# Kernel tuning notes

Measured on AMD Instinct MI355X. Metric: run time of the kernel, lower is better.

Reference implementation:

```python
import jax, jax.numpy as jnp
import numpy as np

B, T, R = 256, 20, 100          # batch, decode steps, image regions
IN_DIM, NUM_HID, V_DIM = 300, 1024, 2048
VOCAB = 10000


def _p(key, shape, scale=0.02):
    return (jax.random.normal(key, shape, dtype=jnp.float32) * scale)


def setup_inputs() -> dict:
    key = jax.random.key(0)
    ks = jax.random.split(key, 24)
    H4 = 4 * NUM_HID
    return {
        "caption": jax.random.randint(ks[0], (B, T - 1), 0, VOCAB),
        "features": jax.random.normal(ks[1], (B, R, V_DIM), dtype=jnp.float32),
        # word embedding table
        "emb": _p(ks[2], (VOCAB, IN_DIM)),
        # v_input: Linear(v_dim, in_dim)
        "W_vin": _p(ks[3], (V_DIM, IN_DIM)), "b_vin": jnp.zeros((IN_DIM,), jnp.float32),
        # rnn_v: LSTMCell(in_dim + num_hid + v_dim, num_hid); weights stored [in, 4H]
        "W_ih_v": _p(ks[4], (IN_DIM + NUM_HID + V_DIM, H4)),
        "W_hh_v": _p(ks[5], (NUM_HID, H4)),
        "b_v": jnp.zeros((H4,), jnp.float32),
        # attention MLP
        "W_va": _p(ks[6], (V_DIM, NUM_HID)), "b_va": jnp.zeros((NUM_HID,), jnp.float32),
        "W_ha": _p(ks[7], (NUM_HID, NUM_HID)), "b_ha": jnp.zeros((NUM_HID,), jnp.float32),
        "W_a": _p(ks[8], (NUM_HID, 1)), "b_a": jnp.zeros((1,), jnp.float32),
        # rnn_c: LSTMCell(num_hid + v_dim, num_hid)
        "W_ih_c": _p(ks[9], (NUM_HID + V_DIM, H4)),
        "W_hh_c": _p(ks[10], (NUM_HID, H4)),
        "b_c": jnp.zeros((H4,), jnp.float32),
        # classifier: Linear(num_hid, vocab)
        "W_cls": _p(ks[11], (NUM_HID, VOCAB)), "b_cls": jnp.zeros((VOCAB,), jnp.float32),
    }


def _lstm_cell(x, h, c, W_ih, W_hh, b):
    # torch LSTMCell gate order: i, f, g, o
    g = x @ W_ih + h @ W_hh + b
    i, f, gg, o = jnp.split(g, 4, axis=-1)
    c2 = jax.nn.sigmoid(f) * c + jax.nn.sigmoid(i) * jnp.tanh(gg)
    h2 = jax.nn.sigmoid(o) * jnp.tanh(c2)
    return h2, c2


def reference(caption, features, emb, W_vin, b_vin, W_ih_v, W_hh_v, b_v,
              W_va, b_va, W_ha, b_ha, W_a, b_a, W_ih_c, W_hh_c, b_c,
              W_cls, b_cls):
    cap_emb = emb[caption]                                  # [B, T-1, in_dim]
    feat_mean = jnp.mean(features, axis=1)                  # [B, v_dim]
    v_rnn_inp = feat_mean @ W_vin + b_vin                   # [B, in_dim]
    x = jnp.concatenate([v_rnn_inp[:, None, :], cap_emb], axis=1)  # [B, T, in_dim]
    # precompute region projection (loop-invariant in the original)
    va = features @ W_va + b_va                             # [B, R, num_hid]

    def step(carry, x_t):
        h_v, c_v, h_c, c_c = carry
        inp_v = jnp.concatenate([feat_mean, h_c, x_t], axis=1)
        h_v, c_v = _lstm_cell(inp_v, h_v, c_v, W_ih_v, W_hh_v, b_v)
        ha = h_v @ W_ha + b_ha                              # [B, num_hid]
        att_logit = jnp.tanh(va + ha[:, None, :]) @ W_a + b_a  # [B, R, 1]
        att = jax.nn.softmax(att_logit, axis=1)             # softmax over regions
        feat_hat = jnp.mean(features * att, axis=1)         # [B, v_dim] (mean, as in torch)
        inp_c = jnp.concatenate([feat_hat, h_v], axis=1)
        h_c, c_c = _lstm_cell(inp_c, h_c, c_c, W_ih_c, W_hh_c, b_c)
        return (h_v, c_v, h_c, c_c), (h_c, att)

    z = jnp.zeros((x.shape[0], NUM_HID), jnp.float32)
    _, (outs, atts) = jax.lax.scan(step, (z, z, z, z), jnp.swapaxes(x, 0, 1))
    outputs = jnp.swapaxes(outs, 0, 1)                      # [B, T, num_hid]
    attention = jnp.swapaxes(atts, 0, 1)                    # [B, T, R, 1]
    repr_ = outputs @ W_cls + b_cls                         # [B, T, vocab]
    return repr_, attention
```

## Files before the change

kernel.cpp:

```cpp
#include <hip/hip_runtime.h>
#include <math.h>

namespace {

constexpr int NB  = 256;
constexpr int NT  = 20;
constexpr int NR  = 100;
constexpr int IND = 300;
constexpr int NH  = 1024;
constexpr int VD  = 2048;
constexpr int H4  = 4096;
constexpr int VOC = 10000;
constexpr int VOCP = 10112;

constexpr int KGV = 4704;  constexpr int KGVO = 2352;
constexpr int KGC = 8192;  constexpr int KGCO = 4096;
constexpr int KHA = 2048;  constexpr int KHAO = 1024;
constexpr int KCL = 2048;  constexpr int KCLO = 1024;
constexpr int KFM = 4096;  constexpr int KFMO = 2048;
constexpr int NVI = 384;
constexpr int A2VLD = 4096;
constexpr int X2LD  = 608;

constexpr int ZGV = 8;  constexpr int KSV = 608;
constexpr int ZGC = 8;  constexpr int KSC = 1024;
constexpr int ZHA = 16; constexpr int KSH = 128;
constexpr int ZFM = 8;  constexpr int KSF = 512;

typedef short  s8v  __attribute__((ext_vector_type(8)));
typedef float  f4v  __attribute__((ext_vector_type(4)));

__device__ __forceinline__ float sigm(float x) { return 1.f / (1.f + expf(-x)); }
__device__ __forceinline__ unsigned short f2b(float x) {
  return __builtin_bit_cast(unsigned short, (__bf16)x);
}
__device__ __forceinline__ float b2f(unsigned short u) {
  return (float)__builtin_bit_cast(__bf16, u);
}
__device__ __forceinline__ int Frow(int row) { return (row ^ (row >> 2)) & 3; }
__device__ __forceinline__ void storeCK(unsigned short* rowbase, int segkp, int korig,
                                        float x, int Fs) {
  const unsigned short h = f2b(x);
  const unsigned short l = f2b(x - b2f(h));
  const int ph = segkp + ((korig >> 3) << 4) + (korig & 7);
  rowbase[ph ^ Fs] = h;
  rowbase[(ph + 8) ^ Fs] = l;
}

__device__ __forceinline__ void gload16(const unsigned short* g, unsigned short* l) {
  __builtin_amdgcn_global_load_lds(
      (const __attribute__((address_space(1))) void*)g,
      (__attribute__((address_space(3))) void*)l, 16, 0, 0);
}

#define BARRIER()  __syncthreads()
#define VMWAIT0()  asm volatile("s_waitcnt vmcnt(0)" ::: "memory")

template<bool OUT_BF16, bool DUPB>
__global__ __launch_bounds__(256)
void gemm128(const unsigned short* __restrict__ A, int lda,
             const unsigned short* __restrict__ Bt, int ldb,
             void* __restrict__ Cv, int ldc,
             const float* __restrict__ bias,
             int N, int Kp)
{
  __shared__ unsigned short As[2][128 * 32];
  __shared__ unsigned short Bs[2][128 * 32];
  const int tid = threadIdx.x, wid = tid >> 6, lane = tid & 63;
  const int wm = (wid >> 1) * 64, wn = (wid & 1) * 64;
  const int m0 = blockIdx.x * 128, n0 = blockIdx.y * 128;
  const int sr = tid >> 2, sc = (tid & 3) * 8;
  const unsigned short* a0 = A + (size_t)(m0 + sr) * lda + sc;
  const unsigned short* a1 = a0 + (size_t)64 * lda;
  const unsigned short* bsrcD = Bt + (size_t)(n0 + (tid >> 1)) * ldb + (tid & 1) * 8;
  const unsigned short* b0 = Bt + (size_t)(n0 + sr) * ldb + sc;
  const unsigned short* b1 = b0 + (size_t)64 * ldb;
  const int rr = lane & 15;
  const int kc = (((lane >> 4) ^ Frow(rr)) & 3) * 8;
  const int wrow = tid >> 1, wc8 = tid & 1;
  const int wF = Frow(wrow & 15);

  f4v acc[4][4] = {};

  auto stageA = [&](int s, int k) {
    gload16(a0 + k, &As[s][tid * 8]);
    gload16(a1 + k, &As[s][2048 + tid * 8]);
  };
  auto stageBplain = [&](int s, int k) {
    gload16(b0 + k, &Bs[s][tid * 8]);
    gload16(b1 + k, &Bs[s][2048 + tid * 8]);
  };
  auto writeBdup = [&](int s, s8v v) {
    *(s8v*)&Bs[s][wrow * 32 + (((2 * wc8) ^ wF) * 8)] = v;
    *(s8v*)&Bs[s][wrow * 32 + (((2 * wc8 + 1) ^ wF) * 8)] = v;
  };
  auto compute = [&](int s) {
    s8v a[4], b[4];
#pragma unroll
    for (int i = 0; i < 4; ++i) a[i] = *(const s8v*)&As[s][(wm + i * 16 + rr) * 32 + kc];
#pragma unroll
    for (int j = 0; j < 4; ++j) b[j] = *(const s8v*)&Bs[s][(wn + j * 16 + rr) * 32 + kc];
#pragma unroll
    for (int i = 0; i < 4; ++i)
#pragma unroll
      for (int j = 0; j < 4; ++j)
        acc[i][j] = __builtin_amdgcn_mfma_f32_16x16x32_bf16(a[i], b[j], acc[i][j], 0, 0, 0);
  };

  stageA(0, 0);
  if constexpr (DUPB) {
    s8v v = *(const s8v*)(bsrcD);
    VMWAIT0();
    writeBdup(0, v);
  } else {
    stageBplain(0, 0);
    VMWAIT0();
  }
  BARRIER();

  int cur = 0;
  for (int k0 = 0; k0 < Kp; k0 += 32) {
    const bool more = (k0 + 32 < Kp);
    if constexpr (DUPB) {
      s8v v;
      if (more) { stageA(cur ^ 1, k0 + 32); v = *(const s8v*)(bsrcD + ((k0 + 32) >> 1)); }
      compute(cur);
      VMWAIT0();
      if (more) writeBdup(cur ^ 1, v);
    } else {
      if (more) { stageA(cur ^ 1, k0 + 32); stageBplain(cur ^ 1, k0 + 32); }
      compute(cur);
      VMWAIT0();
    }
    BARRIER();
    cur ^= 1;
  }

  const int cr = (lane >> 4) * 4, cc = lane & 15;
#pragma unroll
  for (int i = 0; i < 4; ++i) {
#pragma unroll
    for (int j = 0; j < 4; ++j) {
      const int gn = n0 + wn + j * 16 + cc;
      if (gn >= N) continue;
#pragma unroll
      for (int r = 0; r < 4; ++r) {
        const int gm = m0 + wm + i * 16 + cr + r;
        float v = acc[i][j][r] + bias[gn];
        if constexpr (OUT_BF16) ((unsigned short*)Cv)[(size_t)gm * ldc + gn] = f2b(v);
        else                    ((float*)Cv)[(size_t)gm * ldc + gn] = v;
      }
    }
  }
}

template<bool XSEG>
__global__ __launch_bounds__(256)
void gemm_sk2(const unsigned short* __restrict__ A, int lda,
              const unsigned short* __restrict__ X2, int t,
              const unsigned short* __restrict__ Bt, int ldb,
              float* __restrict__ P, int N, int Kp, int Ksplit)
{
  __shared__ unsigned short As[2][128 * 32];
  __shared__ unsigned short Bs[2][128 * 32];
  const int tid = threadIdx.x, wid = tid >> 6, lane = tid & 63;
  const int wm = (wid >> 1) * 64, wn = (wid & 1) * 64;
  const int m0 = blockIdx.y * 128, n0 = blockIdx.x * 128;
  const int kbeg = blockIdx.z * Ksplit;
  const int kend = min(Kp, kbeg + Ksplit);
  const int sr = tid >> 2, sc = (tid & 3) * 8;
  const unsigned short* a0 = A + (size_t)(m0 + sr) * lda + sc;
  const unsigned short* a1 = a0 + (size_t)64 * lda;
  const unsigned short* x0 = nullptr;
  const unsigned short* x1 = nullptr;
  if constexpr (XSEG) {
    x0 = X2 + ((size_t)(m0 + sr) * NT + t) * X2LD + sc;
    x1 = x0 + (size_t)64 * NT * X2LD;
  }
  const unsigned short* bsrcD = Bt + (size_t)(n0 + (tid >> 1)) * ldb + (tid & 1) * 8;
  const int rr = lane & 15;
  const int kc = (((lane >> 4) ^ Frow(rr)) & 3) * 8;
  const int wrow = tid >> 1, wc8 = tid & 1;
  const int wF = Frow(wrow & 15);

  f4v acc[4][4] = {};

  auto stageA = [&](int s, int k) {
    if constexpr (XSEG) {
      if (k >= A2VLD) {
        gload16(x0 + (k - A2VLD), &As[s][tid * 8]);
        gload16(x1 + (k - A2VLD), &As[s][2048 + tid * 8]);
      } else {
        gload16(a0 + k, &As[s][tid * 8]);
        gload16(a1 + k, &As[s][2048 + tid * 8]);
      }
    } else {
      gload16(a0 + k, &As[s][tid * 8]);
      gload16(a1 + k, &As[s][2048 + tid * 8]);
    }
  };
  auto writeBdup = [&](int s, s8v v) {
    *(s8v*)&Bs[s][wrow * 32 + (((2 * wc8) ^ wF) * 8)] = v;
    *(s8v*)&Bs[s][wrow * 32 + (((2 * wc8 + 1) ^ wF) * 8)] = v;
  };
  auto compute = [&](int s) {
    s8v a[4], b[4];
#pragma unroll
    for (int i = 0; i < 4; ++i) a[i] = *(const s8v*)&As[s][(wm + i * 16 + rr) * 32 + kc];
#pragma unroll
    for (int j = 0; j < 4; ++j) b[j] = *(const s8v*)&Bs[s][(wn + j * 16 + rr) * 32 + kc];
#pragma unroll
    for (int i = 0; i < 4; ++i)
#pragma unroll
      for (int j = 0; j < 4; ++j)
        acc[i][j] = __builtin_amdgcn_mfma_f32_16x16x32_bf16(a[i], b[j], acc[i][j], 0, 0, 0);
  };

  stageA(0, kbeg);
  {
    s8v v = *(const s8v*)(bsrcD + (kbeg >> 1));
    VMWAIT0();
    writeBdup(0, v);
  }
  BARRIER();

  int cur = 0;
  for (int k0 = kbeg; k0 < kend; k0 += 32) {
    const bool more = (k0 + 32 < kend);
    s8v v;
    if (more) { stageA(cur ^ 1, k0 + 32); v = *(const s8v*)(bsrcD + ((k0 + 32) >> 1)); }
    compute(cur);
    VMWAIT0();
    if (more) writeBdup(cur ^ 1, v);
    BARRIER();
    cur ^= 1;
  }

  float* out = P + (size_t)blockIdx.z * 256 * N;
  const int cr = (lane >> 4) * 4, cc = lane & 15;
#pragma unroll
  for (int i = 0; i < 4; ++i)
#pragma unroll
    for (int j = 0; j < 4; ++j)
#pragma unroll
      for (int r = 0; r < 4; ++r)
        out[(size_t)(m0 + wm + i * 16 + cr + r) * N + n0 + wn + j * 16 + cc] = acc[i][j][r];
}

__global__ __launch_bounds__(256)
void gemm_va_f32(const float* __restrict__ A, int lda,
                 const unsigned short* __restrict__ Bt, int ldb,
                 unsigned short* __restrict__ C, int ldc,
                 const float* __restrict__ bias, int N, int Kp)
{
  __shared__ unsigned short As[128 * 32];
  __shared__ unsigned short Bs[128 * 32];
  const int tid = threadIdx.x, wid = tid >> 6, lane = tid & 63;
  const int wm = (wid >> 1) * 64, wn = (wid & 1) * 64;
  const int m0 = blockIdx.x * 128, n0 = blockIdx.y * 128;
  const unsigned short* bsrc0 = Bt + (size_t)(n0 + (tid >> 2)) * ldb + (tid & 3) * 8;
  const unsigned short* bsrc1 = bsrc0 + (size_t)64 * ldb;
  const int rr = lane & 15;
  const int kc = (((lane >> 4) ^ Frow(rr)) & 3) * 8;

  f4v acc[4][4] = {};
  for (int k0 = 0; k0 < Kp; k0 += 32) {
#pragma unroll
    for (int it = 0; it < 4; ++it) {
      const int r = it * 32 + (tid >> 3), c = (tid & 7) * 4;
      const float4 v = *(const float4*)(A + (size_t)(m0 + r) * lda + k0 + c);
      ushort4 w;
      w.x = f2b(v.x); w.y = f2b(v.y); w.z = f2b(v.z); w.w = f2b(v.w);
      *(ushort4*)&As[r * 32 + (c ^ (Frow(r & 15) << 3))] = w;
    }
    gload16(bsrc0 + k0, &Bs[tid * 8]);
    gload16(bsrc1 + k0, &Bs[2048 + tid * 8]);
    __syncthreads();
    s8v a[4], b[4];
#pragma unroll
    for (int i = 0; i < 4; ++i) a[i] = *(const s8v*)&As[(wm + i * 16 + rr) * 32 + kc];
#pragma unroll
    for (int j = 0; j < 4; ++j) b[j] = *(const s8v*)&Bs[(wn + j * 16 + rr) * 32 + kc];
#pragma unroll
    for (int i = 0; i < 4; ++i)
#pragma unroll
      for (int j = 0; j < 4; ++j)
        acc[i][j] = __builtin_amdgcn_mfma_f32_16x16x32_bf16(a[i], b[j], acc[i][j], 0, 0, 0);
    __syncthreads();
  }
  const int cr = (lane >> 4) * 4, cc = lane & 15;
#pragma unroll
  for (int i = 0; i < 4; ++i)
#pragma unroll
    for (int j = 0; j < 4; ++j) {
      const int gn = n0 + wn + j * 16 + cc;
      if (gn >= N) continue;
#pragma unroll
      for (int r = 0; r < 4; ++r)
        C[(size_t)(m0 + wm + i * 16 + cr + r) * ldc + gn] = f2b(acc[i][j][r] + bias[gn]);
    }
}

__global__ void convB_k(const float* __restrict__ src, int srcld, int K, int N,
                        unsigned short* __restrict__ dst, int dstld, int coff, int mode)
{
  __shared__ float t[32][33];
  const int kb = blockIdx.x * 32, nb = blockIdx.y * 32;
  const int tx = threadIdx.x & 31, ty = threadIdx.x >> 5;
#pragma unroll
  for (int i = 0; i < 32; i += 8) {
    const int k = kb + ty + i, n = nb + tx;
    t[ty + i][tx] = (k < K && n < N) ? src[(size_t)k * srcld + n] : 0.f;
  }
  __syncthreads();
#pragma unroll
  for (int i = 0; i < 32; i += 8) {
    const int n = nb + ty + i, k = kb + tx;
    if (n >= N || k >= K) continue;
    const float x = t[tx][ty + i];
    unsigned short* row = dst + (size_t)n * dstld;
    if (mode == 0) {
      row[coff + k] = f2b(x);
    } else {
      row[(coff + k) ^ (Frow(n & 15) << 3)] = f2b(x);
    }
  }
}

__global__ void zpad_plain_k(unsigned short* __restrict__ dst, int ld, int c0, int N)
{
  const int w = ld - c0;
  const int idx = blockIdx.x * 256 + threadIdx.x;
  if (idx >= N * w) return;
  dst[(size_t)(idx / w) * ld + c0 + (idx % w)] = 0;
}

__global__ void zfill_k(unsigned short* __restrict__ p, int n)
{
  const int i = blockIdx.x * 256 + threadIdx.x;
  if (i < n) p[i] = 0;
}

__global__ void feat_pass_k(const float* __restrict__ feat, float* __restrict__ fm,
                            unsigned short* __restrict__ f16out)
{
  const int idx = blockIdx.x * 256 + threadIdx.x;
  if (idx >= NB * (VD / 8)) return;
  const int d0 = (idx & (VD / 8 - 1)) * 8, b = idx / (VD / 8);
  const float* base = feat + (size_t)b * NR * VD + d0;
  float s[8] = {};
  for (int r = 0; r < NR; ++r) {
    const float4 x0 = *(const float4*)(base + (size_t)r * VD);
    const float4 x1 = *(const float4*)(base + (size_t)r * VD + 4);
    s[0] += x0.x; s[1] += x0.y; s[2] += x0.z; s[3] += x0.w;
    s[4] += x1.x; s[5] += x1.y; s[6] += x1.z; s[7] += x1.w;
    if (f16out) {
      unsigned short w[8] = {f2b(x0.x), f2b(x0.y), f2b(x0.z), f2b(x0.w),
                             f2b(x1.x), f2b(x1.y), f2b(x1.z), f2b(x1.w)};
      const int ro = b * NR + r;
      *(s8v*)(f16out + (size_t)ro * VD + (d0 ^ (Frow(ro & 15) << 3))) = *(const s8v*)w;
    }
  }
#pragma unroll
  for (int e = 0; e < 8; ++e) fm[(size_t)b * VD + d0 + e] = s[e] * (1.f / NR);
}

__global__ void pack_fm_k(const float* __restrict__ fm, unsigned short* __restrict__ fm2)
{
  const int idx = blockIdx.x * 256 + threadIdx.x;
  if (idx >= NB * VD) return;
  const int k = idx & (VD - 1), b = idx >> 11;
  storeCK(fm2 + (size_t)b * KFM, 0, k, fm[idx], Frow(b & 15) << 3);
}

__global__ void fmg_red_k(const float* __restrict__ gp, const float* __restrict__ bv,
                          float* __restrict__ fmg)
{
  const int idx = blockIdx.x * 256 + threadIdx.x;
  if (idx >= NB * H4) return;
  float s = bv[idx & (H4 - 1)];
#pragma unroll
  for (int z = 0; z < ZFM; ++z) s += gp[(size_t)z * NB * H4 + idx];
  fmg[idx] = s;
}

__global__ void vinp_red_k(const float* __restrict__ gp, const float* __restrict__ bvin,
                           float* __restrict__ vinp)
{
  const int idx = blockIdx.x * 256 + threadIdx.x;
  if (idx >= NB * IND) return;
  const int n = idx % IND, b = idx / IND;
  float s = bvin[n];
#pragma unroll
  for (int z = 0; z < ZFM; ++z) s += gp[(size_t)z * NB * NVI + (size_t)b * NVI + n];
  vinp[idx] = s;
}

__global__ void build_x2_k(const int* __restrict__ cap, const float* __restrict__ emb,
                           const float* __restrict__ vinp, unsigned short* __restrict__ X2)
{
  const int idx = blockIdx.x * 256 + threadIdx.x;
  if (idx >= NB * NT * X2LD) return;
  const int c = idx % X2LD;
  const int bt = idx / X2LD;
  const int t = bt % NT, b = bt / NT;
  const int Fs = Frow(b & 15) << 3;
  const int chunk = c >> 4, sub = (c >> 3) & 1, w = c & 7;
  const int d = chunk * 8 + w;
  unsigned short val = 0;
  if (d < IND) {
    const float v = (t == 0) ? vinp[b * IND + d]
                             : emb[(size_t)cap[b * (NT - 1) + (t - 1)] * IND + d];
    const unsigned short h = f2b(v);
    val = sub ? f2b(v - b2f(h)) : h;
  }
  X2[(size_t)bt * X2LD + (c ^ Fs)] = val;
}

__global__ void lstm_pw_v_k(const float* __restrict__ gp, const float* __restrict__ fmg,
                            float* __restrict__ cv,
                            unsigned short* __restrict__ A2c, unsigned short* __restrict__ A2v)
{
  const int idx = blockIdx.x * 256 + threadIdx.x;
  if (idx >= NB * NH) return;
  const int n = idx & (NH - 1), b = idx >> 10;
  const size_t base = (size_t)b * H4;
  float gi = fmg[base + n], gf = fmg[base + NH + n];
  float gg = fmg[base + 2 * NH + n], go = fmg[base + 3 * NH + n];
#pragma unroll
  for (int z = 0; z < ZGV; ++z) {
    const float* g = gp + (size_t)z * NB * H4 + base;
    gi += g[n]; gf += g[NH + n]; gg += g[2 * NH + n]; go += g[3 * NH + n];
  }
  const float c2 = sigm(gf) * cv[idx] + sigm(gi) * tanhf(gg);
  const float h2 = sigm(go) * tanhf(c2);
  cv[idx] = c2;
  const int Fs = Frow(b & 15) << 3;
  storeCK(A2c + (size_t)b * KGC, 4096, n, h2, Fs);
  storeCK(A2v + (size_t)b * A2VLD, 2048, n, h2, Fs);
}

__global__ void lstm_pw_c_k(const float* __restrict__ gp, const float* __restrict__ bc,
                            float* __restrict__ cc,
                            unsigned short* __restrict__ A2v, unsigned short* __restrict__ A2c,
                            unsigned short* __restrict__ outh2, int t)
{
  const int idx = blockIdx.x * 256 + threadIdx.x;
  if (idx >= NB * NH) return;
  const int n = idx & (NH - 1), b = idx >> 10;
  const size_t base = (size_t)b * H4;
  float gi = bc[n], gf = bc[NH + n], gg = bc[2 * NH + n], go = bc[3 * NH + n];
#pragma unroll
  for (int z = 0; z < ZGC; ++z) {
    const float* g = gp + (size_t)z * NB * H4 + base;
    gi += g[n]; gf += g[NH + n]; gg += g[2 * NH + n]; go += g[3 * NH + n];
  }
  const float c2 = sigm(gf) * cc[idx] + sigm(gi) * tanhf(gg);
  const float h2 = sigm(go) * tanhf(c2);
  cc[idx] = c2;
  const int Fs = Frow(b & 15) << 3;
  storeCK(A2v + (size_t)b * A2VLD, 0, n, h2, Fs);
  storeCK(A2c + (size_t)b * KGC, 6144, n, h2, Fs);
  const int ro = b * NT + t;
  storeCK(outh2 + (size_t)ro * KCL, 0, n, h2, Frow(ro & 15) << 3);
}

template<bool F16>
__global__ __launch_bounds__(512)
void att_fused_k(const unsigned short* __restrict__ va16,
                 const float* __restrict__ hap,
                 const float* __restrict__ bha,
                 const float* __restrict__ Wa, const float* __restrict__ ba,
                 const unsigned short* __restrict__ f16,
                 const float* __restrict__ f32,
                 unsigned short* __restrict__ A2c,
                 float* __restrict__ att_out, int t)
{
  const int b = blockIdx.x, tid = threadIdx.x;
  const int lane = tid & 63, wid = tid >> 6;
  __shared__ float ha_s[NH];
  __shared__ float wa_s[NH];
  __shared__ float red_s[128];
  __shared__ float fh_s[2][VD];

  for (int j = tid; j < NH; j += 512) {
    float s = bha[j];
#pragma unroll
    for (int z = 0; z < ZHA; ++z) s += hap[((size_t)z * NB + b) * NH + j];
    ha_s[j] = s;
    wa_s[j] = Wa[j];
  }
  __syncthreads();

  for (int r = wid; r < NR; r += 8) {
    const unsigned short* vrow = va16 + ((size_t)b * NR + r) * NH + lane * 16;
    float s = 0.f;
#pragma unroll
    for (int u = 0; u < 2; ++u) {
      const s8v v = *(const s8v*)(vrow + u * 8);
      const int j0 = lane * 16 + u * 8;
#pragma unroll
      for (int e = 0; e < 8; ++e)
        s += tanhf(b2f((unsigned short)v[e]) + ha_s[j0 + e]) * wa_s[j0 + e];
    }
    for (int o = 32; o; o >>= 1) s += __shfl_down(s, o);
    if (lane == 0) red_s[r] = s + ba[0];
  }
  __syncthreads();

  if (wid == 0) {
    float v0 = (lane < NR) ? red_s[lane] : -3.4e38f;
    float v1 = (lane + 64 < NR) ? red_s[lane + 64] : -3.4e38f;
    float m = fmaxf(v0, v1);
    for (int o = 32; o; o >>= 1) m = fmaxf(m, __shfl_xor(m, o));
    const float e0 = (lane < NR) ? expf(v0 - m) : 0.f;
    const float e1 = (lane + 64 < NR) ? expf(v1 - m) : 0.f;
    float s = e0 + e1;
    for (int o = 32; o; o >>= 1) s += __shfl_xor(s, o);
    const float inv = 1.f / s;
    if (lane < NR) red_s[lane] = e0 * inv;
    if (lane + 64 < NR) red_s[lane + 64] = e1 * inv;
  }
  __syncthreads();
  if (tid < NR) att_out[((size_t)b * NT + t) * NR + tid] = red_s[tid];

  const int half = tid >> 8;
  const int dd = (tid & 255) * 8;
  const int r0 = half * 50, r1 = r0 + 50;
  float fh8[8] = {};
  if constexpr (F16) {
    const unsigned short* fbase = f16 + (size_t)b * NR * VD;
    for (int r = r0; r < r1; ++r) {
      const int ro = b * NR + r;
      const s8v f = *(const s8v*)(fbase + (size_t)r * VD + (dd ^ (Frow(ro & 15) << 3)));
      const float a = red_s[r];
#pragma unroll
      for (int e = 0; e < 8; ++e) fh8[e] += a * b2f((unsigned short)f[e]);
    }
  } else {
    const float* fb = f32 + (size_t)b * NR * VD + dd;
    for (int r = r0; r < r1; ++r) {
      const float4 x0 = *(const float4*)(fb + (size_t)r * VD);
      const float4 x1 = *(const float4*)(fb + (size_t)r * VD + 4);
      const float a = red_s[r];
      fh8[0] += a * x0.x; fh8[1] += a * x0.y; fh8[2] += a * x0.z; fh8[3] += a * x0.w;
      fh8[4] += a * x1.x; fh8[5] += a * x1.y; fh8[6] += a * x1.z; fh8[7] += a * x1.w;
    }
  }
#pragma unroll
  for (int e = 0; e < 8; ++e) fh_s[half][dd + e] = fh8[e];
  __syncthreads();

  unsigned short* rowbase = A2c + (size_t)b * KGC;
  const int Fs = Frow(b & 15) << 3;
  const int d0 = tid * 4;
#pragma unroll
  for (int e = 0; e < 4; ++e) {
    const float v = (fh_s[0][d0 + e] + fh_s[1][d0 + e]) * (1.f / NR);
    storeCK(rowbase, 0, d0 + e, v, Fs);
  }
}

inline void convB(hipStream_t st, const float* src, int srcld, int K, int N,
                  unsigned short* dst, int dstld, int coff, int mode)
{
  dim3 g((K + 31) / 32, (N + 31) / 32);
  convB_k<<<g, 256, 0, st>>>(src, srcld, K, N, dst, dstld, coff, mode);
}

}

extern "C" void kernel_launch(void* const* d_in, const int* in_sizes, int n_in,
                              void* d_out, int out_size, void* d_ws, size_t ws_size,
                              hipStream_t stream)
{
  const int*   caption = (const int*)  d_in[0];
  const float* feat    = (const float*)d_in[1];
  const float* emb     = (const float*)d_in[2];
  const float* W_vin   = (const float*)d_in[3];
  const float* b_vin   = (const float*)d_in[4];
  const float* W_ih_v  = (const float*)d_in[5];
  const float* W_hh_v  = (const float*)d_in[6];
  const float* b_v     = (const float*)d_in[7];
  const float* W_va    = (const float*)d_in[8];
  const float* b_va    = (const float*)d_in[9];
  const float* W_ha    = (const float*)d_in[10];
  const float* b_ha    = (const float*)d_in[11];
  const float* W_a     = (const float*)d_in[12];
  const float* b_a     = (const float*)d_in[13];
  const float* W_ih_c  = (const float*)d_in[14];
  const float* W_hh_c  = (const float*)d_in[15];
  const float* b_c     = (const float*)d_in[16];
  const float* W_cls   = (const float*)d_in[17];
  const float* b_cls   = (const float*)d_in[18];

  float* out_repr = (float*)d_out;
  float* out_att  = out_repr + (size_t)NB * NT * VOC;

  char* cur = (char*)d_ws;
  auto take = [&](size_t bytes) { char* p = cur; cur += bytes; return p; };

  unsigned short* A2v  = (unsigned short*)take((size_t)NB * A2VLD * 2);
  unsigned short* A2c  = (unsigned short*)take((size_t)NB * KGC * 2);
  float* CV            = (float*)take((size_t)NB * NH * 4);
  float* CC            = (float*)take((size_t)NB * NH * 4);
  const size_t ZERO_BYTES = (size_t)NB * A2VLD * 2 + (size_t)NB * KGC * 2
                          + 2 * (size_t)NB * NH * 4;

  float* FM            = (float*)take((size_t)NB * VD * 4);
  float* VINP          = (float*)take((size_t)NB * IND * 4);
  unsigned short* X2   = (unsigned short*)take((size_t)NB * NT * X2LD * 2);
  float* FMG           = (float*)take((size_t)NB * H4 * 4);
  unsigned short* FM2  = (unsigned short*)take((size_t)NB * KFM * 2);
  unsigned short* VA16 = (unsigned short*)take((size_t)NB * NR * NH * 2);
  float* GP            = (float*)take((size_t)ZGC * NB * H4 * 4);
  float* HAP           = (float*)take((size_t)ZHA * NB * NH * 4);
  unsigned short* OUTH2= (unsigned short*)take((size_t)NB * NT * KCL * 2);
  unsigned short* Wgv2t= (unsigned short*)take((size_t)H4 * KGVO * 2);
  unsigned short* Wha2t= (unsigned short*)take((size_t)NH * KHAO * 2);
  unsigned short* Wgc2t= (unsigned short*)take((size_t)H4 * KGCO * 2);
  unsigned short* Wfmg = (unsigned short*)take((size_t)H4 * KFMO * 2);
  unsigned short* WvinT= (unsigned short*)take((size_t)NVI * KFMO * 2);
  unsigned short* Wcls2t=(unsigned short*)take((size_t)VOCP * KCLO * 2);
  unsigned short* Wva16t=(unsigned short*)take((size_t)NH * VD * 2);
  unsigned short* FEAT16=(unsigned short*)cur;
  const bool useF16 = ((size_t)(cur - (char*)d_ws) + (size_t)NB * NR * VD * 2) <= ws_size;

  hipMemsetAsync(A2v, 0, ZERO_BYTES, stream);

  convB(stream, W_ih_v + (size_t)2048 * H4, H4, 1024, H4, Wgv2t, KGVO, 0,    0);
  convB(stream, W_hh_v,                     H4, 1024, H4, Wgv2t, KGVO, 1024, 0);
  convB(stream, W_ih_v + (size_t)3072 * H4, H4, 300,  H4, Wgv2t, KGVO, 2048, 0);
  zpad_plain_k<<<((H4 * (KGVO - 2348)) + 255) / 256, 256, 0, stream>>>(
      Wgv2t, KGVO, 2348, H4);
  convB(stream, W_ha, NH, 1024, NH, Wha2t, KHAO, 0, 0);
  convB(stream, W_ih_c,                     H4, 2048, H4, Wgc2t, KGCO, 0,    0);
  convB(stream, W_ih_c + (size_t)2048 * H4, H4, 1024, H4, Wgc2t, KGCO, 2048, 0);
  convB(stream, W_hh_c,                     H4, 1024, H4, Wgc2t, KGCO, 3072, 0);
  convB(stream, W_ih_v,                     H4, 2048, H4, Wfmg,  KFMO, 0,    0);
  convB(stream, W_vin, IND, 2048, IND, WvinT, KFMO, 0, 0);
  zfill_k<<<(((NVI - IND) * KFMO) + 255) / 256, 256, 0, stream>>>(
      WvinT + (size_t)IND * KFMO, (NVI - IND) * KFMO);
  convB(stream, W_cls, VOC, 1024, VOC, Wcls2t, KCLO, 0, 0);
  zfill_k<<<(((VOCP - VOC) * KCLO) + 255) / 256, 256, 0, stream>>>(
      Wcls2t + (size_t)VOC * KCLO, (VOCP - VOC) * KCLO);
  convB(stream, W_va, NH, VD, NH, Wva16t, VD, 0, 1);

  feat_pass_k<<<(NB * (VD / 8) + 255) / 256, 256, 0, stream>>>(
      feat, FM, useF16 ? FEAT16 : nullptr);
  pack_fm_k<<<(NB * VD + 255) / 256, 256, 0, stream>>>(FM, FM2);
  gemm_sk2<false><<<dim3(NVI / 128, 2, ZFM), 256, 0, stream>>>(
      FM2, KFM, nullptr, 0, WvinT, KFMO, GP, NVI, KFM, KSF);
  vinp_red_k<<<(NB * IND + 255) / 256, 256, 0, stream>>>(GP, b_vin, VINP);
  build_x2_k<<<(NB * NT * X2LD + 255) / 256, 256, 0, stream>>>(caption, emb, VINP, X2);
  gemm_sk2<false><<<dim3(H4 / 128, 2, ZFM), 256, 0, stream>>>(
      FM2, KFM, nullptr, 0, Wfmg, KFMO, GP, H4, KFM, KSF);
  fmg_red_k<<<(NB * H4 + 255) / 256, 256, 0, stream>>>(GP, b_v, FMG);
  if (useF16) {
    dim3 g((NB * NR) / 128, NH / 128);
    gemm128<true, false><<<g, 256, 0, stream>>>(
        FEAT16, VD, Wva16t, VD, VA16, NH, b_va, NH, VD);
  } else {
    dim3 g((NB * NR) / 128, NH / 128);
    gemm_va_f32<<<g, 256, 0, stream>>>(feat, VD, Wva16t, VD, VA16, NH, b_va, NH, VD);
  }

  for (int t = 0; t < NT; ++t) {
    gemm_sk2<true><<<dim3(H4 / 128, 2, ZGV), 256, 0, stream>>>(
        A2v, A2VLD, X2, t, Wgv2t, KGVO, GP, H4, KGV, KSV);
    lstm_pw_v_k<<<(NB * NH + 255) / 256, 256, 0, stream>>>(GP, FMG, CV, A2c, A2v);
    gemm_sk2<false><<<dim3(NH / 128, 2, ZHA), 256, 0, stream>>>(
        A2c + 4096, KGC, nullptr, 0, Wha2t, KHAO, HAP, NH, KHA, KSH);
    if (useF16)
      att_fused_k<true><<<NB, 512, 0, stream>>>(
          VA16, HAP, b_ha, W_a, b_a, FEAT16, nullptr, A2c, out_att, t);
    else
      att_fused_k<false><<<NB, 512, 0, stream>>>(
          VA16, HAP, b_ha, W_a, b_a, nullptr, feat, A2c, out_att, t);
    gemm_sk2<false><<<dim3(H4 / 128, 2, ZGC), 256, 0, stream>>>(
        A2c, KGC, nullptr, 0, Wgc2t, KGCO, GP, H4, KGC, KSC);
    lstm_pw_c_k<<<(NB * NH + 255) / 256, 256, 0, stream>>>(GP, b_c, CC, A2v, A2c, OUTH2, t);
  }

  {
    dim3 g((NB * NT) / 128, VOCP / 128);
    gemm128<false, true><<<g, 256, 0, stream>>>(
        OUTH2, KCL, Wcls2t, KCLO, out_repr, VOC, b_cls, VOC, KCL);
  }
}
```

Measured before the change: 3.347 ms.

## Drop split-bf16 hi/lo compensation for recurrent GEMM activations, halve K

Recurrent LSTM and attention GEMM activations were stored as bf16 hi+lo pairs with each weight duplicated, which doubled the K dimension. They are now stored as a single bf16 value. K, the split sizes and the buffer strides are halved, and weights are now swizzled so B tiles load straight into LDS through global_load_lds instead of passing through registers with duplication. This cuts GEMM work and weight bandwidth in every timestep, at the cost of lower activation precision, which may affect accuracy tolerance. The classifier path keeps the compensated form.

Measured after the change: 2.861 ms. 14.5% less time.

```diff
diff --git a/kernel.cpp b/kernel.cpp
--- a/kernel.cpp
+++ b/kernel.cpp
@@ -13,19 +13,19 @@
 constexpr int VOC = 10000;
 constexpr int VOCP = 10112;
 
-constexpr int KGV = 4704;  constexpr int KGVO = 2352;
-constexpr int KGC = 8192;  constexpr int KGCO = 4096;
-constexpr int KHA = 2048;  constexpr int KHAO = 1024;
+constexpr int KGV = 2368;
+constexpr int KGC = 4096;
+constexpr int KHA = 1024;
 constexpr int KCL = 2048;  constexpr int KCLO = 1024;
-constexpr int KFM = 4096;  constexpr int KFMO = 2048;
+constexpr int KFM = 2048;
 constexpr int NVI = 384;
-constexpr int A2VLD = 4096;
-constexpr int X2LD  = 608;
-
-constexpr int ZGV = 8;  constexpr int KSV = 608;
-constexpr int ZGC = 8;  constexpr int KSC = 1024;
-constexpr int ZHA = 16; constexpr int KSH = 128;
-constexpr int ZFM = 8;  constexpr int KSF = 512;
+constexpr int A2VLD = 2048;
+constexpr int X2LD  = 320;
+
+constexpr int ZGV = 8;  constexpr int KSV = 320;
+constexpr int ZGC = 8;  constexpr int KSC = 512;
+constexpr int ZHA = 8;  constexpr int KSH = 128;
+constexpr int ZFM = 8;  constexpr int KSF = 256;
 
 typedef short  s8v  __attribute__((ext_vector_type(8)));
 typedef float  f4v  __attribute__((ext_vector_type(4)));
@@ -38,11 +38,13 @@
   return (float)__builtin_bit_cast(__bf16, u);
 }
 __device__ __forceinline__ int Frow(int row) { return (row ^ (row >> 2)) & 3; }
-__device__ __forceinline__ void storeCK(unsigned short* rowbase, int segkp, int korig,
-                                        float x, int Fs) {
+__device__ __forceinline__ void store1(unsigned short* rowbase, int k, float x, int Fs) {
+  rowbase[k ^ Fs] = f2b(x);
+}
+__device__ __forceinline__ void storeCK(unsigned short* rowbase, int korig, float x, int Fs) {
   const unsigned short h = f2b(x);
   const unsigned short l = f2b(x - b2f(h));
-  const int ph = segkp + ((korig >> 3) << 4) + (korig & 7);
+  const int ph = ((korig >> 3) << 4) + (korig & 7);
   rowbase[ph ^ Fs] = h;
   rowbase[(ph + 8) ^ Fs] = l;
 }
@@ -177,15 +179,14 @@
     x0 = X2 + ((size_t)(m0 + sr) * NT + t) * X2LD + sc;
     x1 = x0 + (size_t)64 * NT * X2LD;
   }
-  const unsigned short* bsrcD = Bt + (size_t)(n0 + (tid >> 1)) * ldb + (tid & 1) * 8;
+  const unsigned short* b0 = Bt + (size_t)(n0 + sr) * ldb + sc;
+  const unsigned short* b1 = b0 + (size_t)64 * ldb;
   const int rr = lane & 15;
   const int kc = (((lane >> 4) ^ Frow(rr)) & 3) * 8;
-  const int wrow = tid >> 1, wc8 = tid & 1;
-  const int wF = Frow(wrow & 15);
 
   f4v acc[4][4] = {};
 
-  auto stageA = [&](int s, int k) {
+  auto stage = [&](int s, int k) {
     if constexpr (XSEG) {
       if (k >= A2VLD) {
         gload16(x0 + (k - A2VLD), &As[s][tid * 8]);
@@ -198,10 +199,8 @@
       gload16(a0 + k, &As[s][tid * 8]);
       gload16(a1 + k, &As[s][2048 + tid * 8]);
     }
-  };
-  auto writeBdup = [&](int s, s8v v) {
-    *(s8v*)&Bs[s][wrow * 32 + (((2 * wc8) ^ wF) * 8)] = v;
-    *(s8v*)&Bs[s][wrow * 32 + (((2 * wc8 + 1) ^ wF) * 8)] = v;
+    gload16(b0 + k, &Bs[s][tid * 8]);
+    gload16(b1 + k, &Bs[s][2048 + tid * 8]);
   };
   auto compute = [&](int s) {
     s8v a[4], b[4];
@@ -216,22 +215,15 @@
         acc[i][j] = __builtin_amdgcn_mfma_f32_16x16x32_bf16(a[i], b[j], acc[i][j], 0, 0, 0);
   };
 
-  stageA(0, kbeg);
-  {
-    s8v v = *(const s8v*)(bsrcD + (kbeg >> 1));
-    VMWAIT0();
-    writeBdup(0, v);
-  }
+  stage(0, kbeg);
+  VMWAIT0();
   BARRIER();
 
   int cur = 0;
   for (int k0 = kbeg; k0 < kend; k0 += 32) {
-    const bool more = (k0 + 32 < kend);
-    s8v v;
-    if (more) { stageA(cur ^ 1, k0 + 32); v = *(const s8v*)(bsrcD + ((k0 + 32) >> 1)); }
+    if (k0 + 32 < kend) stage(cur ^ 1, k0 + 32);
     compute(cur);
     VMWAIT0();
-    if (more) writeBdup(cur ^ 1, v);
     BARRIER();
     cur ^= 1;
   }
@@ -327,12 +319,13 @@
   }
 }
 
-__global__ void zpad_plain_k(unsigned short* __restrict__ dst, int ld, int c0, int N)
+__global__ void zpad_swz_k(unsigned short* __restrict__ dst, int ld, int c0, int N)
 {
   const int w = ld - c0;
   const int idx = blockIdx.x * 256 + threadIdx.x;
   if (idx >= N * w) return;
-  dst[(size_t)(idx / w) * ld + c0 + (idx % w)] = 0;
+  const int n = idx / w, c = c0 + (idx % w);
+  dst[(size_t)n * ld + (c ^ (Frow(n & 15) << 3))] = 0;
 }
 
 __global__ void zfill_k(unsigned short* __restrict__ p, int n)
@@ -341,7 +334,8 @@
   if (i < n) p[i] = 0;
 }
 
-__global__ void feat_pass_k(const float* __restrict__ feat, float* __restrict__ fm,
+__global__ void feat_pass_k(const float* __restrict__ feat,
+                            unsigned short* __restrict__ fm16,
                             unsigned short* __restrict__ f16out)
 {
   const int idx = blockIdx.x * 256 + threadIdx.x;
@@ -361,16 +355,10 @@
       *(s8v*)(f16out + (size_t)ro * VD + (d0 ^ (Frow(ro & 15) << 3))) = *(const s8v*)w;
     }
   }
-#pragma unroll
-  for (int e = 0; e < 8; ++e) fm[(size_t)b * VD + d0 + e] = s[e] * (1.f / NR);
-}
-
-__global__ void pack_fm_k(const float* __restrict__ fm, unsigned short* __restrict__ fm2)
-{
-  const int idx = blockIdx.x * 256 + threadIdx.x;
-  if (idx >= NB * VD) return;
-  const int k = idx & (VD - 1), b = idx >> 11;
-  storeCK(fm2 + (size_t)b * KFM, 0, k, fm[idx], Frow(b & 15) << 3);
+  unsigned short w[8];
+#pragma unroll
+  for (int e = 0; e < 8; ++e) w[e] = f2b(s[e] * (1.f / NR));
+  *(s8v*)(fm16 + (size_t)b * KFM + (d0 ^ (Frow(b & 15) << 3))) = *(const s8v*)w;
 }
 
 __global__ void fmg_red_k(const float* __restrict__ gp, const float* __restrict__ bv,
@@ -405,14 +393,11 @@
   const int bt = idx / X2LD;
   const int t = bt % NT, b = bt / NT;
   const int Fs = Frow(b & 15) << 3;
-  const int chunk = c >> 4, sub = (c >> 3) & 1, w = c & 7;
-  const int d = chunk * 8 + w;
   unsigned short val = 0;
-  if (d < IND) {
-    const float v = (t == 0) ? vinp[b * IND + d]
-                             : emb[(size_t)cap[b * (NT - 1) + (t - 1)] * IND + d];
-    const unsigned short h = f2b(v);
-    val = sub ? f2b(v - b2f(h)) : h;
+  if (c < IND) {
+    const float v = (t == 0) ? vinp[b * IND + c]
+                             : emb[(size_t)cap[b * (NT - 1) + (t - 1)] * IND + c];
+    val = f2b(v);
   }
   X2[(size_t)bt * X2LD + (c ^ Fs)] = val;
 }
@@ -436,8 +421,8 @@
   const float h2 = sigm(go) * tanhf(c2);
   cv[idx] = c2;
   const int Fs = Frow(b & 15) << 3;
-  storeCK(A2c + (size_t)b * KGC, 4096, n, h2, Fs);
-  storeCK(A2v + (size_t)b * A2VLD, 2048, n, h2, Fs);
+  store1(A2c + (size_t)b * KGC, 2048 + n, h2, Fs);
+  store1(A2v + (size_t)b * A2VLD, 1024 + n, h2, Fs);
 }
 
 __global__ void lstm_pw_c_k(const float* __restrict__ gp, const float* __restrict__ bc,
@@ -459,10 +444,10 @@
   const float h2 = sigm(go) * tanhf(c2);
   cc[idx] = c2;
   const int Fs = Frow(b & 15) << 3;
-  storeCK(A2v + (size_t)b * A2VLD, 0, n, h2, Fs);
-  storeCK(A2c + (size_t)b * KGC, 6144, n, h2, Fs);
+  store1(A2v + (size_t)b * A2VLD, n, h2, Fs);
+  store1(A2c + (size_t)b * KGC, 3072 + n, h2, Fs);
   const int ro = b * NT + t;
-  storeCK(outh2 + (size_t)ro * KCL, 0, n, h2, Frow(ro & 15) << 3);
+  storeCK(outh2 + (size_t)ro * KCL, n, h2, Frow(ro & 15) << 3);
 }
 
 template<bool F16>
@@ -557,7 +542,7 @@
 #pragma unroll
   for (int e = 0; e < 4; ++e) {
     const float v = (fh_s[0][d0 + e] + fh_s[1][d0 + e]) * (1.f / NR);
-    storeCK(rowbase, 0, d0 + e, v, Fs);
+    store1(rowbase, d0 + e, v, Fs);
   }
 }
 
@@ -607,20 +592,19 @@
   const size_t ZERO_BYTES = (size_t)NB * A2VLD * 2 + (size_t)NB * KGC * 2
                           + 2 * (size_t)NB * NH * 4;
 
-  float* FM            = (float*)take((size_t)NB * VD * 4);
   float* VINP          = (float*)take((size_t)NB * IND * 4);
   unsigned short* X2   = (unsigned short*)take((size_t)NB * NT * X2LD * 2);
   float* FMG           = (float*)take((size_t)NB * H4 * 4);
-  unsigned short* FM2  = (unsigned short*)take((size_t)NB * KFM * 2);
+  unsigned short* FM16 = (unsigned short*)take((size_t)NB * KFM * 2);
   unsigned short* VA16 = (unsigned short*)take((size_t)NB * NR * NH * 2);
   float* GP            = (float*)take((size_t)ZGC * NB * H4 * 4);
   float* HAP           = (float*)take((size_t)ZHA * NB * NH * 4);
   unsigned short* OUTH2= (unsigned short*)take((size_t)NB * NT * KCL * 2);
-  unsigned short* Wgv2t= (unsigned short*)take((size_t)H4 * KGVO * 2);
-  unsigned short* Wha2t= (unsigned short*)take((size_t)NH * KHAO * 2);
-  unsigned short* Wgc2t= (unsigned short*)take((size_t)H4 * KGCO * 2);
-  unsigned short* Wfmg = (unsigned short*)take((size_t)H4 * KFMO * 2);
-  unsigned short* WvinT= (unsigned short*)take((size_t)NVI * KFMO * 2);
+  unsigned short* Wgv2t= (unsigned short*)take((size_t)H4 * KGV * 2);
+  unsigned short* Wha2t= (unsigned short*)take((size_t)NH * KHA * 2);
+  unsigned short* Wgc2t= (unsigned short*)take((size_t)H4 * KGC * 2);
+  unsigned short* Wfmg = (unsigned short*)take((size_t)H4 * KFM * 2);
+  unsigned short* WvinT= (unsigned short*)take((size_t)NVI * KFM * 2);
   unsigned short* Wcls2t=(unsigned short*)take((size_t)VOCP * KCLO * 2);
   unsigned short* Wva16t=(unsigned short*)take((size_t)NH * VD * 2);
   unsigned short* FEAT16=(unsigned short*)cur;
@@ -628,33 +612,32 @@
 
   hipMemsetAsync(A2v, 0, ZERO_BYTES, stream);
 
-  convB(stream, W_ih_v + (size_t)2048 * H4, H4, 1024, H4, Wgv2t, KGVO, 0,    0);
-  convB(stream, W_hh_v,                     H4, 1024, H4, Wgv2t, KGVO, 1024, 0);
-  convB(stream, W_ih_v + (size_t)3072 * H4, H4, 300,  H4, Wgv2t, KGVO, 2048, 0);
-  zpad_plain_k<<<((H4 * (KGVO - 2348)) + 255) / 256, 256, 0, stream>>>(
-      Wgv2t, KGVO, 2348, H4);
-  convB(stream, W_ha, NH, 1024, NH, Wha2t, KHAO, 0, 0);
-  convB(stream, W_ih_c,                     H4, 2048, H4, Wgc2t, KGCO, 0,    0);
-  convB(stream, W_ih_c + (size_t)2048 * H4, H4, 1024, H4, Wgc2t, KGCO, 2048, 0);
-  convB(stream, W_hh_c,                     H4, 1024, H4, Wgc2t, KGCO, 3072, 0);
-  convB(stream, W_ih_v,                     H4, 2048, H4, Wfmg,  KFMO, 0,    0);
-  convB(stream, W_vin, IND, 2048, IND, WvinT, KFMO, 0, 0);
-  zfill_k<<<(((NVI - IND) * KFMO) + 255) / 256, 256, 0, stream>>>(
-      WvinT + (size_t)IND * KFMO, (NVI - IND) * KFMO);
+  convB(stream, W_ih_v + (size_t)2048 * H4, H4, 1024, H4, Wgv2t, KGV, 0,    1);
+  convB(stream, W_hh_v,                     H4, 1024, H4, Wgv2t, KGV, 1024, 1);
+  convB(stream, W_ih_v + (size_t)3072 * H4, H4, 300,  H4, Wgv2t, KGV, 2048, 1);
+  zpad_swz_k<<<((H4 * (KGV - 2348)) + 255) / 256, 256, 0, stream>>>(
+      Wgv2t, KGV, 2348, H4);
+  convB(stream, W_ha, NH, 1024, NH, Wha2t, KHA, 0, 1);
+  convB(stream, W_ih_c,                     H4, 2048, H4, Wgc2t, KGC, 0,    1);
+  convB(stream, W_ih_c + (size_t)2048 * H4, H4, 1024, H4, Wgc2t, KGC, 2048, 1);
+  convB(stream, W_hh_c,                     H4, 1024, H4, Wgc2t, KGC, 3072, 1);
+  convB(stream, W_ih_v,                     H4, 2048, H4, Wfmg,  KFM, 0,    1);
+  convB(stream, W_vin, IND, 2048, IND, WvinT, KFM, 0, 1);
+  zfill_k<<<(((NVI - IND) * KFM) + 255) / 256, 256, 0, stream>>>(
+      WvinT + (size_t)IND * KFM, (NVI - IND) * KFM);
   convB(stream, W_cls, VOC, 1024, VOC, Wcls2t, KCLO, 0, 0);
   zfill_k<<<(((VOCP - VOC) * KCLO) + 255) / 256, 256, 0, stream>>>(
       Wcls2t + (size_t)VOC * KCLO, (VOCP - VOC) * KCLO);
   convB(stream, W_va, NH, VD, NH, Wva16t, VD, 0, 1);
 
   feat_pass_k<<<(NB * (VD / 8) + 255) / 256, 256, 0, stream>>>(
-      feat, FM, useF16 ? FEAT16 : nullptr);
-  pack_fm_k<<<(NB * VD + 255) / 256, 256, 0, stream>>>(FM, FM2);
+      feat, FM16, useF16 ? FEAT16 : nullptr);
   gemm_sk2<false><<<dim3(NVI / 128, 2, ZFM), 256, 0, stream>>>(
-      FM2, KFM, nullptr, 0, WvinT, KFMO, GP, NVI, KFM, KSF);
+      FM16, KFM, nullptr, 0, WvinT, KFM, GP, NVI, KFM, KSF);
   vinp_red_k<<<(NB * IND + 255) / 256, 256, 0, stream>>>(GP, b_vin, VINP);
   build_x2_k<<<(NB * NT * X2LD + 255) / 256, 256, 0, stream>>>(caption, emb, VINP, X2);
   gemm_sk2<false><<<dim3(H4 / 128, 2, ZFM), 256, 0, stream>>>(
-      FM2, KFM, nullptr, 0, Wfmg, KFMO, GP, H4, KFM, KSF);
+      FM16, KFM, nullptr, 0, Wfmg, KFM, GP, H4, KFM, KSF);
   fmg_red_k<<<(NB * H4 + 255) / 256, 256, 0, stream>>>(GP, b_v, FMG);
   if (useF16) {
     dim3 g((NB * NR) / 128, NH / 128);
@@ -667,10 +650,10 @@
 
   for (int t = 0; t < NT; ++t) {
     gemm_sk2<true><<<dim3(H4 / 128, 2, ZGV), 256, 0, stream>>>(
-        A2v, A2VLD, X2, t, Wgv2t, KGVO, GP, H4, KGV, KSV);
+        A2v, A2VLD, X2, t, Wgv2t, KGV, GP, H4, KGV, KSV);
     lstm_pw_v_k<<<(NB * NH + 255) / 256, 256, 0, stream>>>(GP, FMG, CV, A2c, A2v);
     gemm_sk2<false><<<dim3(NH / 128, 2, ZHA), 256, 0, stream>>>(
-        A2c + 4096, KGC, nullptr, 0, Wha2t, KHAO, HAP, NH, KHA, KSH);
+        A2c + 2048, KGC, nullptr, 0, Wha2t, KHA, HAP, NH, KHA, KSH);
     if (useF16)
       att_fused_k<true><<<NB, 512, 0, stream>>>(
           VA16, HAP, b_ha, W_a, b_a, FEAT16, nullptr, A2c, out_att, t);
@@ -678,7 +661,7 @@
       att_fused_k<false><<<NB, 512, 0, stream>>>(
           VA16, HAP, b_ha, W_a, b_a, nullptr, feat, A2c, out_att, t);
     gemm_sk2<false><<<dim3(H4 / 128, 2, ZGC), 256, 0, stream>>>(
-        A2c, KGC, nullptr, 0, Wgc2t, KGCO, GP, H4, KGC, KSC);
+        A2c, KGC, nullptr, 0, Wgc2t, KGC, GP, H4, KGC, KSC);
     lstm_pw_c_k<<<(NB * NH + 255) / 256, 256, 0, stream>>>(GP, b_c, CC, A2v, A2c, OUTH2, t);
   }
 
```
